# Kernel optimization log

Measured on AMD Instinct MI355X. Metric: run time of the kernel, lower is better.

## Reference

```python
import jax, jax.numpy as jnp
import numpy as np
import math

B, S, D, H = 2, 2048, 4096, 32
HD = D // H  # 128


def setup_inputs() -> dict:
    key = jax.random.key(0)
    ks = jax.random.split(key, 8)
    x = jax.random.normal(ks[0], (B, S, D), dtype=jnp.float32)
    wq = jax.random.normal(ks[1], (D, D), dtype=jnp.float32) * 0.02
    wk = jax.random.normal(ks[2], (D, D), dtype=jnp.float32) * 0.02
    wv = jax.random.normal(ks[3], (D, D), dtype=jnp.float32) * 0.02
    wo = jax.random.normal(ks[4], (D, D), dtype=jnp.float32) * 0.02
    # RoPE frequencies as in LLaMA: theta = 10000^{-2i/hd}
    inv_freq = 1.0 / (10000.0 ** (np.arange(0, HD, 2, dtype=np.float32) / HD))  # [HD/2]
    t = np.arange(S, dtype=np.float32)
    freqs = np.outer(t, inv_freq)  # [S, HD/2]
    freqs_cos = jnp.asarray(np.cos(freqs))
    freqs_sin = jnp.asarray(np.sin(freqs))
    # additive causal mask [1,1,S,S]
    neg = jnp.full((S, S), -1e9, dtype=jnp.float32)
    mask = jnp.triu(neg, k=1)[None, None, :, :]
    return {"x": x, "wq": wq, "wk": wk, "wv": wv, "wo": wo,
            "freqs_cos": freqs_cos, "freqs_sin": freqs_sin, "mask": mask}


def _apply_rope(t, cos, sin):
    # t: [b, s, h, hd]; cos/sin: [s, hd/2]. Complex mult on (even, odd) pairs.
    tr = t.reshape(*t.shape[:-1], HD // 2, 2)
    xr, xi = tr[..., 0], tr[..., 1]
    c = cos[None, :, None, :]
    s = sin[None, :, None, :]
    out_r = xr * c - xi * s
    out_i = xr * s + xi * c
    return jnp.stack([out_r, out_i], axis=-1).reshape(t.shape)


def reference(x, wq, wk, wv, wo, freqs_cos, freqs_sin, mask):
    b, s, d = x.shape
    # projections (nn.Linear: y = x @ W^T)
    xq = (x @ wq.T).reshape(b, s, H, HD)
    xk = (x @ wk.T).reshape(b, s, H, HD)
    xv = (x @ wv.T).reshape(b, s, H, HD)
    xq = _apply_rope(xq, freqs_cos, freqs_sin)
    xk = _apply_rope(xk, freqs_cos, freqs_sin)
    # [b,h,q,k] scores, softmax in fp32, then attend
    scores = jnp.einsum('bqhd,bkhd->bhqk', xq, xk) / math.sqrt(HD)
    scores = scores + mask
    probs = jax.nn.softmax(scores.astype(jnp.float32), axis=-1).astype(xq.dtype)
    out = jnp.einsum('bhqk,bkhd->bqhd', probs, xv).reshape(b, s, d)
    return out @ wo.T
```

## Files before the change

kernel.cpp:

```cpp
#include <hip/hip_runtime.h>

typedef __bf16 bf16x8 __attribute__((ext_vector_type(8)));
typedef float f32x4 __attribute__((ext_vector_type(4)));
typedef float f32x16 __attribute__((ext_vector_type(16)));
typedef unsigned short u16;
typedef unsigned int u32;
typedef u16 u16x8 __attribute__((ext_vector_type(8)));
typedef u16 u16x4 __attribute__((ext_vector_type(4)));
typedef u32 u32x4 __attribute__((ext_vector_type(4)));

#define B_ 2
#define S_ 2048
#define D_ 4096
#define H_ 32
#define HD_ 128
#define SM_SCALE 0.08838834764831845f
#define C2_ 0.12751743f

__device__ __forceinline__ u16 f2bf(float f) {
  __bf16 h = (__bf16)f;
  return __builtin_bit_cast(unsigned short, h);
}
__device__ __forceinline__ float bf2f(u16 u) {
  return (float)__builtin_bit_cast(__bf16, u);
}

#define GLD_TO_LDS16(gsrc, ldst)                                                     \
  __builtin_amdgcn_global_load_lds((__attribute__((address_space(1))) void*)(gsrc),  \
                                   (__attribute__((address_space(3))) void*)(ldst),  \
                                   16, 0, 0)

__global__ __launch_bounds__(256) void cvt5_kernel(const float* __restrict__ s0,
                                                   const float* __restrict__ s1,
                                                   const float* __restrict__ s2,
                                                   const float* __restrict__ s3,
                                                   const float* __restrict__ s4,
                                                   u16* __restrict__ d0,
                                                   u16* __restrict__ d1,
                                                   u16* __restrict__ d2,
                                                   u16* __restrict__ d3,
                                                   u16* __restrict__ d4,
                                                   int n4) {
  const int region = blockIdx.x >> 9;
  const float* src = region == 0 ? s0 : region == 1 ? s1 : region == 2 ? s2
                   : region == 3 ? s3 : s4;
  u16* dst = region == 0 ? d0 : region == 1 ? d1 : region == 2 ? d2
           : region == 3 ? d3 : d4;
  int i = (blockIdx.x & 511) * 256 + threadIdx.x;
  const int stride = 512 * 256;
  for (; i < n4; i += stride) {
    float4 v = reinterpret_cast<const float4*>(src)[i];
    u16x4 o;
    o[0] = f2bf(v.x); o[1] = f2bf(v.y); o[2] = f2bf(v.z); o[3] = f2bf(v.w);
    reinterpret_cast<u16x4*>(dst)[i] = o;
  }
}


#define LGKM0()                                            \
  do {                                                     \
    asm volatile("s_waitcnt lgkmcnt(0)" ::: "memory");     \
    __builtin_amdgcn_sched_barrier(0);                     \
  } while (0)

__device__ __forceinline__ void fill_aq(bf16x8 (&dst)[2][4], const u16* half_base,
                                        int wr, int lane) {
#pragma unroll
  for (int ks = 0; ks < 2; ++ks)
#pragma unroll
    for (int m = 0; m < 4; ++m) {
      int rr = wr * 64 + m * 16 + (lane & 15);
      int c8 = (ks * 4 + (lane >> 4)) ^ (rr & 7);
      dst[ks][m] = *reinterpret_cast<const bf16x8*>(half_base + rr * 64 + c8 * 8);
    }
}
__device__ __forceinline__ void fill_bq(bf16x8 (&dst)[2][2], const u16* half_base,
                                        int wn, int lane) {
#pragma unroll
  for (int ks = 0; ks < 2; ++ks)
#pragma unroll
    for (int n = 0; n < 2; ++n) {
      int rr = wn * 32 + n * 16 + (lane & 15);
      int c8 = (ks * 4 + (lane >> 4)) ^ (rr & 7);
      dst[ks][n] = *reinterpret_cast<const bf16x8*>(half_base + rr * 64 + c8 * 8);
    }
}

#define MFMA16(MQ, NQ, AF, BF)                                                   \
  do {                                                                           \
    __builtin_amdgcn_s_setprio(1);                                               \
    _Pragma("unroll") for (int ks = 0; ks < 2; ++ks)                             \
      _Pragma("unroll") for (int m = 0; m < 4; ++m)                              \
        _Pragma("unroll") for (int n = 0; n < 2; ++n)                            \
          acc[(MQ) * 4 + m][(NQ) * 2 + n] =                                      \
              __builtin_amdgcn_mfma_f32_16x16x32_bf16(                           \
                  (AF)[ks][m], (BF)[ks][n], acc[(MQ) * 4 + m][(NQ) * 2 + n],     \
                  0, 0, 0);                                                      \
    __builtin_amdgcn_s_setprio(0);                                               \
  } while (0)

template <typename OutT, bool ROPE>
__global__ __launch_bounds__(512, 2) void gemm256_kernel(const u16* __restrict__ A,
                                                         const u16* __restrict__ Bw,
                                                         OutT* __restrict__ C,
                                                         int M, int N, int K,
                                                         const float* __restrict__ fc,
                                                         const float* __restrict__ fs) {
  __shared__ u16 As[2][2][8192];
  __shared__ u16 Bs[2][2][8192];
  const int tid = threadIdx.x;
  const int lane = tid & 63;
  const int w = tid >> 6;
  const int wr = w >> 2;
  const int wn = w & 3;
  const int nbx = N >> 8;
  const int nby = M >> 8;
  const int nwg = nby * nbx;
  int tr, tc;
  if (nby == 16 && nbx == 16) {
    int xcd = blockIdx.x & 7, j = blockIdx.x >> 3;
    tr = (xcd >> 1) * 4 + (j >> 3);
    tc = (xcd & 1) * 8 + (j & 7);
  } else {
    int wg = blockIdx.x;
    if ((nwg & 7) == 0) wg = (wg & 7) * (nwg >> 3) + (wg >> 3);
    tr = wg / nbx; tc = wg % nbx;
  }

  const size_t arow0 = (size_t)tr * 256;
  const size_t brow0 = (size_t)tc * 256;
  const int KT = K >> 6;

  auto stageA = [&](int t, int half) {
    if (t >= KT) return;
    const int k0 = t << 6;
    u16* base = &As[t & 1][half][0];
#pragma unroll
    for (int i = 0; i < 2; ++i) {
      int q = i * 512 + tid;
      int r = q >> 3;
      int c8 = (q & 7) ^ (r & 7);
      GLD_TO_LDS16(A + (arow0 + half * 128 + r) * K + k0 + c8 * 8, base + q * 8);
    }
  };
  auto stageB = [&](int t, int half) {
    if (t >= KT) return;
    const int k0 = t << 6;
    u16* base = &Bs[t & 1][half][0];
#pragma unroll
    for (int i = 0; i < 2; ++i) {
      int q = i * 512 + tid;
      int r = q >> 3;
      int c8 = (q & 7) ^ (r & 7);
      GLD_TO_LDS16(Bw + (brow0 + half * 128 + r) * K + k0 + c8 * 8, base + q * 8);
    }
  };

  f32x4 acc[8][4] = {};
  bf16x8 aF[2][4], bF0[2][2], bF1[2][2];

  stageA(0, 0); stageB(0, 0); stageA(0, 1); stageB(0, 1);
  stageA(1, 0); stageB(1, 0);
  asm volatile("s_waitcnt vmcnt(4)" ::: "memory");
  __builtin_amdgcn_s_barrier();
  __builtin_amdgcn_sched_barrier(0);

  for (int t = 0; t < KT; ++t) {
    const int buf = t & 1;
    const u16* Ah0 = &As[buf][0][0];
    const u16* Ah1 = &As[buf][1][0];
    const u16* Bh0 = &Bs[buf][0][0];
    const u16* Bh1 = &Bs[buf][1][0];

    fill_aq(aF, Ah0, wr, lane);
    fill_bq(bF0, Bh0, wn, lane);
    stageA(t + 1, 1);
    __builtin_amdgcn_s_barrier();
    LGKM0();
    MFMA16(0, 0, aF, bF0);
    __builtin_amdgcn_s_barrier();

    fill_bq(bF1, Bh1, wn, lane);
    stageB(t + 1, 1);
    __builtin_amdgcn_s_barrier();
    LGKM0();
    MFMA16(0, 1, aF, bF1);
    __builtin_amdgcn_s_barrier();

    fill_aq(aF, Ah1, wr, lane);
    stageA(t + 2, 0);
    __builtin_amdgcn_s_barrier();
    LGKM0();
    MFMA16(1, 0, aF, bF0);
    __builtin_amdgcn_s_barrier();

    stageB(t + 2, 0);
    if (t >= KT - 2) asm volatile("s_waitcnt vmcnt(0)" ::: "memory");
    else             asm volatile("s_waitcnt vmcnt(4)" ::: "memory");
    __builtin_amdgcn_s_barrier();
    __builtin_amdgcn_sched_barrier(0);
    MFMA16(1, 1, aF, bF1);
    __builtin_amdgcn_s_barrier();
  }

#pragma unroll
  for (int mi = 0; mi < 8; ++mi) {
    const int mq = mi >> 2, m = mi & 3;
#pragma unroll
    for (int ni = 0; ni < 4; ++ni) {
      const int nq = ni >> 1, n = ni & 1;
#pragma unroll
      for (int r = 0; r < 4; ++r) {
        size_t row = arow0 + mq * 128 + wr * 64 + m * 16 + ((lane >> 4) << 2) + r;
        size_t col = (size_t)tc * 256 + nq * 128 + wn * 32 + n * 16 + (lane & 15);
        float v = acc[mi][ni][r];
        if constexpr (ROPE) {
          float o = __shfl_xor(v, 1);
          int s = (int)(row & (S_ - 1));
          int p = (wn * 32 + n * 16 + (lane & 14)) >> 1;
          float cv = fc[(s << 6) + p];
          float sv = fs[(s << 6) + p];
          v = (lane & 1) ? (v * cv + o * sv) : (v * cv - o * sv);
        }
        if constexpr (__is_same(OutT, float)) {
          C[row * N + col] = v;
        } else {
          C[row * N + col] = f2bf(v);
        }
      }
    }
  }
}

__global__ __launch_bounds__(512, 2) void attn_kernel(const u16* __restrict__ Q,
                                                      const u16* __restrict__ K,
                                                      const u16* __restrict__ V,
                                                      u16* __restrict__ O) {
  __shared__ u16 Ks[2][64 * 128];
  __shared__ u16 Vt[2][128 * 64];

  const int blk = blockIdx.x;
  const int pr = blk >> 6;
  const int bh = blk & 63;
  const int b = bh >> 5, h = bh & 31;
  const int tid = threadIdx.x, lane = tid & 63, w = tid >> 6;
  const int l31 = lane & 31;
  const int hi = lane >> 5;
  const int r0 = lane >> 1;
  const int dc = 2 * w + (lane & 1);
  const int vd0 = dc * 8;

  for (int ph = 0; ph < 2; ++ph) {
    const int qt = ph == 0 ? 7 - pr : pr;
    const int q0 = qt << 8;
    const int wq0 = q0 + w * 32;
    const int qg = wq0 + l31;

    bf16x8 qf[8];
#pragma unroll
    for (int kb = 0; kb < 8; ++kb)
      qf[kb] = *reinterpret_cast<const bf16x8*>(Q + (size_t)(b * S_ + qg) * D_ + h * HD_ + kb * 16 + hi * 8);

    f32x16 oacc[4] = {};
    float mrun = -__builtin_inff(), lrun = 0.f;

    const int ntiles = 4 * qt + 4;
    u16x8 vr0, vr1;

    {
#pragma unroll
      for (int it = 0; it < 2; ++it) {
        int ff = it * 512 + tid;
        int row = ff >> 4, cc = ff & 15;
        int scc = cc ^ (row & 7);
        GLD_TO_LDS16(K + (size_t)(b * S_ + row) * D_ + h * HD_ + scc * 8, &Ks[0][ff << 3]);
      }
      vr0 = *reinterpret_cast<const u16x8*>(V + (size_t)(b * S_ + 2 * r0) * D_ + h * HD_ + vd0);
      vr1 = *reinterpret_cast<const u16x8*>(V + (size_t)(b * S_ + 2 * r0 + 1) * D_ + h * HD_ + vd0);
      u32* vt32 = reinterpret_cast<u32*>(&Vt[0][0]);
#pragma unroll
      for (int j = 0; j < 8; ++j) {
        int d = vd0 + j;
        u32 val = (u32)vr0[j] | ((u32)vr1[j] << 16);
        vt32[d * 32 + ((r0 >> 2) ^ j) * 4 + (r0 & 3)] = val;
      }
    }
    __syncthreads();

    for (int t = 0; t < ntiles; ++t) {
      const int cur = t & 1, nxt = cur ^ 1;
      const bool pre = (t + 1 < ntiles);
      if (pre) {
        const int kv1 = (t + 1) << 6;
#pragma unroll
        for (int it = 0; it < 2; ++it) {
          int ff = it * 512 + tid;
          int row = ff >> 4, cc = ff & 15;
          int scc = cc ^ (row & 7);
          GLD_TO_LDS16(K + (size_t)(b * S_ + kv1 + row) * D_ + h * HD_ + scc * 8, &Ks[nxt][ff << 3]);
        }
        vr0 = *reinterpret_cast<const u16x8*>(V + (size_t)(b * S_ + kv1 + 2 * r0) * D_ + h * HD_ + vd0);
        vr1 = *reinterpret_cast<const u16x8*>(V + (size_t)(b * S_ + kv1 + 2 * r0 + 1) * D_ + h * HD_ + vd0);
      }

      const int kv0 = t << 6;
      if (kv0 <= wq0 + 31) {
        f32x16 st[2] = {};
        __builtin_amdgcn_s_setprio(1);
#pragma unroll
        for (int kvh = 0; kvh < 2; ++kvh) {
#pragma unroll
          for (int kb = 0; kb < 8; ++kb) {
            int row = kvh * 32 + l31;
            int cc = (2 * kb + hi) ^ (row & 7);
            bf16x8 kf = *reinterpret_cast<const bf16x8*>(&Ks[cur][(row << 7) + (cc << 3)]);
            st[kvh] = __builtin_amdgcn_mfma_f32_32x32x16_bf16(kf, qf[kb], st[kvh], 0, 0, 0);
          }
        }
        __builtin_amdgcn_s_setprio(0);

        if (kv0 + 63 > wq0) {
#pragma unroll
          for (int kvh = 0; kvh < 2; ++kvh)
#pragma unroll
            for (int r = 0; r < 16; ++r) {
              int kvg = kv0 + kvh * 32 + (r & 3) + 8 * (r >> 2) + 4 * hi;
              if (kvg > qg) st[kvh][r] = -1e30f;
            }
        }

        float vmax = -1e30f;
#pragma unroll
        for (int kvh = 0; kvh < 2; ++kvh)
#pragma unroll
          for (int r = 0; r < 16; ++r) vmax = fmaxf(vmax, st[kvh][r]);
        vmax = fmaxf(vmax, __shfl_xor(vmax, 32));
        if (!__all(vmax <= mrun + 64.0f)) {
          float mnew = fmaxf(mrun, vmax);
          float sc = exp2f((mrun - mnew) * C2_);
          mrun = mnew;
          lrun *= sc;
#pragma unroll
          for (int db = 0; db < 4; ++db)
#pragma unroll
            for (int r = 0; r < 16; ++r) oacc[db][r] *= sc;
        }
        float psum = 0.f;
#pragma unroll
        for (int kvh = 0; kvh < 2; ++kvh)
#pragma unroll
          for (int r = 0; r < 16; ++r) {
            float p = exp2f((st[kvh][r] - mrun) * C2_);
            st[kvh][r] = p;
            psum += p;
          }
        psum += __shfl_xor(psum, 32);
        lrun += psum;

        __builtin_amdgcn_s_setprio(1);
#pragma unroll
        for (int h2 = 0; h2 < 2; ++h2)
#pragma unroll
          for (int s2 = 0; s2 < 2; ++s2) {
            const int rb = s2 * 8;
            u32 w0, w1, w2, w3;
            asm("v_cvt_pk_bf16_f32 %0, %1, %2" : "=v"(w0) : "v"(st[h2][rb + 0]), "v"(st[h2][rb + 1]));
            asm("v_cvt_pk_bf16_f32 %0, %1, %2" : "=v"(w1) : "v"(st[h2][rb + 2]), "v"(st[h2][rb + 3]));
            asm("v_cvt_pk_bf16_f32 %0, %1, %2" : "=v"(w2) : "v"(st[h2][rb + 4]), "v"(st[h2][rb + 5]));
            asm("v_cvt_pk_bf16_f32 %0, %1, %2" : "=v"(w3) : "v"(st[h2][rb + 6]), "v"(st[h2][rb + 7]));
            u32 sw0 = (u32)__shfl_xor((int)w0, 32);
            u32 sw1 = (u32)__shfl_xor((int)w1, 32);
            u32 sw2 = (u32)__shfl_xor((int)w2, 32);
            u32 sw3 = (u32)__shfl_xor((int)w3, 32);
            u32x4 fw;
            fw[0] = hi ? sw2 : w0;
            fw[1] = hi ? sw3 : w1;
            fw[2] = hi ? w2 : sw0;
            fw[3] = hi ? w3 : sw1;
            bf16x8 pfrag = __builtin_bit_cast(bf16x8, fw);
#pragma unroll
            for (int db = 0; db < 4; ++db) {
              int d = db * 32 + l31;
              int cc = (h2 * 4 + s2 * 2 + hi) ^ (d & 7);
              bf16x8 va = *reinterpret_cast<const bf16x8*>(&Vt[cur][(d << 6) + (cc << 3)]);
              oacc[db] = __builtin_amdgcn_mfma_f32_32x32x16_bf16(va, pfrag, oacc[db], 0, 0, 0);
            }
          }
        __builtin_amdgcn_s_setprio(0);
      }

      if (pre) {
        u32* vt32 = reinterpret_cast<u32*>(&Vt[nxt][0]);
#pragma unroll
        for (int j = 0; j < 8; ++j) {
          int d = vd0 + j;
          u32 val = (u32)vr0[j] | ((u32)vr1[j] << 16);
          vt32[d * 32 + ((r0 >> 2) ^ j) * 4 + (r0 & 3)] = val;
        }
      }
      __syncthreads();
    }

    const float rinv = 1.0f / lrun;
#pragma unroll
    for (int db = 0; db < 4; ++db)
#pragma unroll
      for (int g = 0; g < 4; ++g) {
        u16x4 o4;
#pragma unroll
        for (int j = 0; j < 4; ++j) o4[j] = f2bf(oacc[db][g * 4 + j] * rinv);
        int d = db * 32 + g * 8 + 4 * hi;
        *reinterpret_cast<u16x4*>(O + (size_t)(b * S_ + qg) * D_ + h * HD_ + d) = o4;
      }
  }
}

extern "C" void kernel_launch(void* const* d_in, const int* in_sizes, int n_in,
                              void* d_out, int out_size, void* d_ws, size_t ws_size,
                              hipStream_t stream) {
  const float* x = (const float*)d_in[0];
  const float* wq = (const float*)d_in[1];
  const float* wk = (const float*)d_in[2];
  const float* wv = (const float*)d_in[3];
  const float* wo = (const float*)d_in[4];
  const float* fc = (const float*)d_in[5];
  const float* fs = (const float*)d_in[6];
  float* out = (float*)d_out;

  const size_t SLOT = (size_t)B_ * S_ * D_;
  u16* ws = (u16*)d_ws;
  u16* wqb = ws + 0 * SLOT;
  u16* wkb = ws + 1 * SLOT;
  u16* wvb = ws + 2 * SLOT;
  u16* wob = ws + 3 * SLOT;
  u16* xb  = ws + 4 * SLOT;
  u16* Qb  = ws + 5 * SLOT;
  u16* Kb  = ws + 6 * SLOT;
  u16* Vb  = ws + 7 * SLOT;
  u16* Ob  = xb;

  const int n4 = (int)(SLOT / 4);
  cvt5_kernel<<<2560, 256, 0, stream>>>(x, wq, wk, wv, wo, xb, wqb, wkb, wvb, wob, n4);

  gemm256_kernel<u16, true><<<256, 512, 0, stream>>>(xb, wqb, Qb, B_ * S_, D_, D_, fc, fs);
  gemm256_kernel<u16, true><<<256, 512, 0, stream>>>(xb, wkb, Kb, B_ * S_, D_, D_, fc, fs);
  gemm256_kernel<u16, false><<<256, 512, 0, stream>>>(xb, wvb, Vb, B_ * S_, D_, D_, fc, fs);

  attn_kernel<<<256, 512, 0, stream>>>(Qb, Kb, Vb, Ob);

  gemm256_kernel<float, false><<<256, 512, 0, stream>>>(Ob, wob, out, B_ * S_, D_, D_, fc, fs);
}
```

Baseline: 669.6 us.

## Fuse Q/K/V projections into one 768-block GEMM launch with BK=32 tiles

Replaces the three separate Q, K and V projection GEMM launches with a single kernel of 768 workgroups. Each workgroup picks its projection from the block index, relying on the contiguous workspace layout of the weights and outputs. The new kernel uses a K-step of 32 with half the LDS (a smaller swizzle and a different staging schedule), which could allow more resident blocks. The aim is to remove launch gaps and the tail underutilization of 256-block grids on a 256-CU device. The output GEMM is de-templated and keeps its old path.

```diff
diff --git a/kernel.cpp b/kernel.cpp
--- a/kernel.cpp
+++ b/kernel.cpp
@@ -16,6 +16,7 @@
 #define HD_ 128
 #define SM_SCALE 0.08838834764831845f
 #define C2_ 0.12751743f
+#define SLOT_ ((size_t)B_ * S_ * D_)
 
 __device__ __forceinline__ u16 f2bf(float f) {
   __bf16 h = (__bf16)f;
@@ -56,12 +57,149 @@
   }
 }
 
-
 #define LGKM0()                                            \
   do {                                                     \
     asm volatile("s_waitcnt lgkmcnt(0)" ::: "memory");     \
     __builtin_amdgcn_sched_barrier(0);                     \
   } while (0)
+
+
+__device__ __forceinline__ void fill_a32(bf16x8 (&dst)[4], const u16* Ab,
+                                         int wr, int lane, int mq) {
+#pragma unroll
+  for (int m = 0; m < 4; ++m) {
+    int rr = mq * 128 + wr * 64 + m * 16 + (lane & 15);
+    int c = (lane >> 4) ^ ((rr >> 1) & 3);
+    dst[m] = *reinterpret_cast<const bf16x8*>(Ab + rr * 32 + c * 8);
+  }
+}
+__device__ __forceinline__ void fill_b32(bf16x8 (&dst)[2], const u16* Bb,
+                                         int wn, int lane, int nq) {
+#pragma unroll
+  for (int n = 0; n < 2; ++n) {
+    int rr = nq * 128 + wn * 32 + n * 16 + (lane & 15);
+    int c = (lane >> 4) ^ ((rr >> 1) & 3);
+    dst[n] = *reinterpret_cast<const bf16x8*>(Bb + rr * 32 + c * 8);
+  }
+}
+
+#define MFMA8Q(MQ, NQ, A4, B2)                                                   \
+  do {                                                                           \
+    _Pragma("unroll") for (int m = 0; m < 4; ++m)                                \
+      _Pragma("unroll") for (int n = 0; n < 2; ++n)                              \
+        acc[(MQ) * 4 + m][(NQ) * 2 + n] =                                        \
+            __builtin_amdgcn_mfma_f32_16x16x32_bf16(                             \
+                (A4)[m], (B2)[n], acc[(MQ) * 4 + m][(NQ) * 2 + n], 0, 0, 0);     \
+  } while (0)
+
+__global__ __launch_bounds__(512, 2) void gemmqkv_kernel(const u16* __restrict__ A,
+                                                         const u16* __restrict__ W0,
+                                                         u16* __restrict__ C0,
+                                                         const float* __restrict__ fc,
+                                                         const float* __restrict__ fs) {
+  __shared__ u16 As[2][8192];
+  __shared__ u16 Bs[2][8192];
+  const int tid = threadIdx.x;
+  const int lane = tid & 63;
+  const int w = tid >> 6;
+  const int wr = w >> 2;
+  const int wn = w & 3;
+  const int proj = blockIdx.x >> 8;
+  const int inner = blockIdx.x & 255;
+  const int xcd = inner & 7, j = inner >> 3;
+  const int tr = (xcd >> 1) * 4 + (j >> 3);
+  const int tc = (xcd & 1) * 8 + (j & 7);
+
+  const u16* Bw = W0 + (size_t)proj * SLOT_;
+  u16* C = C0 + (size_t)proj * SLOT_;
+  const int K = D_;
+  const size_t arow0 = (size_t)tr * 256;
+  const size_t brow0 = (size_t)tc * 256;
+  const int KT = K >> 5;
+
+  auto stageA = [&](int t, int half) {
+    if (t >= KT) return;
+    const int k0 = t << 5;
+    u16* base = &As[t & 1][half * 4096];
+    int r = tid >> 2, c4 = tid & 3;
+    int cc = c4 ^ ((r >> 1) & 3);
+    GLD_TO_LDS16(A + (arow0 + half * 128 + r) * K + k0 + cc * 8, base + tid * 8);
+  };
+  auto stageB = [&](int t, int half) {
+    if (t >= KT) return;
+    const int k0 = t << 5;
+    u16* base = &Bs[t & 1][half * 4096];
+    int r = tid >> 2, c4 = tid & 3;
+    int cc = c4 ^ ((r >> 1) & 3);
+    GLD_TO_LDS16(Bw + (brow0 + half * 128 + r) * K + k0 + cc * 8, base + tid * 8);
+  };
+
+  f32x4 acc[8][4] = {};
+  bf16x8 aF[4], bF0[2], bF1[2];
+
+  stageA(0, 0); stageA(0, 1); stageB(0, 0); stageB(0, 1);
+  stageA(1, 0); stageB(1, 0); stageB(1, 1);
+  asm volatile("s_waitcnt vmcnt(3)" ::: "memory");
+  __builtin_amdgcn_s_barrier();
+  __builtin_amdgcn_sched_barrier(0);
+
+  for (int t = 0; t < KT; ++t) {
+    const int buf = t & 1;
+    const u16* Ab = &As[buf][0];
+    const u16* Bb = &Bs[buf][0];
+
+    fill_a32(aF, Ab, wr, lane, 0);
+    fill_b32(bF0, Bb, wn, lane, 0);
+    fill_b32(bF1, Bb, wn, lane, 1);
+    stageA(t + 1, 1);
+    __builtin_amdgcn_s_barrier();
+    LGKM0();
+    __builtin_amdgcn_s_setprio(1);
+    MFMA8Q(0, 0, aF, bF0);
+    MFMA8Q(0, 1, aF, bF1);
+    __builtin_amdgcn_s_setprio(0);
+    __builtin_amdgcn_s_barrier();
+
+    fill_a32(aF, Ab, wr, lane, 1);
+    stageA(t + 2, 0);
+    stageB(t + 2, 0);
+    stageB(t + 2, 1);
+    if (t >= KT - 3) asm volatile("s_waitcnt vmcnt(0)" ::: "memory");
+    else             asm volatile("s_waitcnt vmcnt(3)" ::: "memory");
+    __builtin_amdgcn_s_barrier();
+    LGKM0();
+    __builtin_amdgcn_s_setprio(1);
+    MFMA8Q(1, 0, aF, bF0);
+    MFMA8Q(1, 1, aF, bF1);
+    __builtin_amdgcn_s_setprio(0);
+    __builtin_amdgcn_s_barrier();
+  }
+
+  const bool rope = (proj < 2);
+#pragma unroll
+  for (int mi = 0; mi < 8; ++mi) {
+    const int mq = mi >> 2, m = mi & 3;
+#pragma unroll
+    for (int ni = 0; ni < 4; ++ni) {
+      const int nq = ni >> 1, n = ni & 1;
+#pragma unroll
+      for (int r = 0; r < 4; ++r) {
+        size_t row = arow0 + mq * 128 + wr * 64 + m * 16 + ((lane >> 4) << 2) + r;
+        size_t col = (size_t)tc * 256 + nq * 128 + wn * 32 + n * 16 + (lane & 15);
+        float v = acc[mi][ni][r];
+        float o = __shfl_xor(v, 1);
+        if (rope) {
+          int s = (int)(row & (S_ - 1));
+          int p = (wn * 32 + n * 16 + (lane & 14)) >> 1;
+          float cv = fc[(s << 6) + p];
+          float sv = fs[(s << 6) + p];
+          v = (lane & 1) ? (v * cv + o * sv) : (v * cv - o * sv);
+        }
+        C[row * D_ + col] = f2bf(v);
+      }
+    }
+  }
+}
 
 __device__ __forceinline__ void fill_aq(bf16x8 (&dst)[2][4], const u16* half_base,
                                         int wr, int lane) {
@@ -99,13 +237,10 @@
     __builtin_amdgcn_s_setprio(0);                                               \
   } while (0)
 
-template <typename OutT, bool ROPE>
 __global__ __launch_bounds__(512, 2) void gemm256_kernel(const u16* __restrict__ A,
                                                          const u16* __restrict__ Bw,
-                                                         OutT* __restrict__ C,
-                                                         int M, int N, int K,
-                                                         const float* __restrict__ fc,
-                                                         const float* __restrict__ fs) {
+                                                         float* __restrict__ C,
+                                                         int M, int N, int K) {
   __shared__ u16 As[2][2][8192];
   __shared__ u16 Bs[2][2][8192];
   const int tid = threadIdx.x;
@@ -113,19 +248,9 @@
   const int w = tid >> 6;
   const int wr = w >> 2;
   const int wn = w & 3;
-  const int nbx = N >> 8;
-  const int nby = M >> 8;
-  const int nwg = nby * nbx;
-  int tr, tc;
-  if (nby == 16 && nbx == 16) {
-    int xcd = blockIdx.x & 7, j = blockIdx.x >> 3;
-    tr = (xcd >> 1) * 4 + (j >> 3);
-    tc = (xcd & 1) * 8 + (j & 7);
-  } else {
-    int wg = blockIdx.x;
-    if ((nwg & 7) == 0) wg = (wg & 7) * (nwg >> 3) + (wg >> 3);
-    tr = wg / nbx; tc = wg % nbx;
-  }
+  int xcd = blockIdx.x & 7, j = blockIdx.x >> 3;
+  const int tr = (xcd >> 1) * 4 + (j >> 3);
+  const int tc = (xcd & 1) * 8 + (j & 7);
 
   const size_t arow0 = (size_t)tr * 256;
   const size_t brow0 = (size_t)tc * 256;
@@ -213,20 +338,7 @@
       for (int r = 0; r < 4; ++r) {
         size_t row = arow0 + mq * 128 + wr * 64 + m * 16 + ((lane >> 4) << 2) + r;
         size_t col = (size_t)tc * 256 + nq * 128 + wn * 32 + n * 16 + (lane & 15);
-        float v = acc[mi][ni][r];
-        if constexpr (ROPE) {
-          float o = __shfl_xor(v, 1);
-          int s = (int)(row & (S_ - 1));
-          int p = (wn * 32 + n * 16 + (lane & 14)) >> 1;
-          float cv = fc[(s << 6) + p];
-          float sv = fs[(s << 6) + p];
-          v = (lane & 1) ? (v * cv + o * sv) : (v * cv - o * sv);
-        }
-        if constexpr (__is_same(OutT, float)) {
-          C[row * N + col] = v;
-        } else {
-          C[row * N + col] = f2bf(v);
-        }
+        C[row * N + col] = acc[mi][ni][r];
       }
     }
   }
@@ -427,26 +539,23 @@
   const float* fs = (const float*)d_in[6];
   float* out = (float*)d_out;
 
-  const size_t SLOT = (size_t)B_ * S_ * D_;
   u16* ws = (u16*)d_ws;
-  u16* wqb = ws + 0 * SLOT;
-  u16* wkb = ws + 1 * SLOT;
-  u16* wvb = ws + 2 * SLOT;
-  u16* wob = ws + 3 * SLOT;
-  u16* xb  = ws + 4 * SLOT;
-  u16* Qb  = ws + 5 * SLOT;
-  u16* Kb  = ws + 6 * SLOT;
-  u16* Vb  = ws + 7 * SLOT;
+  u16* wqb = ws + 0 * SLOT_;
+  u16* wkb = ws + 1 * SLOT_;
+  u16* wvb = ws + 2 * SLOT_;
+  u16* wob = ws + 3 * SLOT_;
+  u16* xb  = ws + 4 * SLOT_;
+  u16* Qb  = ws + 5 * SLOT_;
+  u16* Kb  = ws + 6 * SLOT_;
+  u16* Vb  = ws + 7 * SLOT_;
   u16* Ob  = xb;
 
-  const int n4 = (int)(SLOT / 4);
+  const int n4 = (int)(SLOT_ / 4);
   cvt5_kernel<<<2560, 256, 0, stream>>>(x, wq, wk, wv, wo, xb, wqb, wkb, wvb, wob, n4);
 
-  gemm256_kernel<u16, true><<<256, 512, 0, stream>>>(xb, wqb, Qb, B_ * S_, D_, D_, fc, fs);
-  gemm256_kernel<u16, true><<<256, 512, 0, stream>>>(xb, wkb, Kb, B_ * S_, D_, D_, fc, fs);
-  gemm256_kernel<u16, false><<<256, 512, 0, stream>>>(xb, wvb, Vb, B_ * S_, D_, D_, fc, fs);
+  gemmqkv_kernel<<<768, 512, 0, stream>>>(xb, wqb, Qb, fc, fs);
 
   attn_kernel<<<256, 512, 0, stream>>>(Qb, Kb, Vb, Ob);
 
-  gemm256_kernel<float, false><<<256, 512, 0, stream>>>(Ob, wob, out, B_ * S_, D_, D_, fc, fs);
-}
+  gemm256_kernel<<<256, 512, 0, stream>>>(Ob, wob, out, B_ * S_, D_, D_);
+}
```

Result: slower. 792.7 us (+18.4%).
